# Optimization experiments

Measured on AMD Instinct MI355X. Metric: run time of the kernel, lower is better.

Reference implementation:

```python
import jax, jax.numpy as jnp
import numpy as np

N_NODES = 100000
N_EDGES = 1600000
D_IN = 128
D_HID = 128
D_OUT = 10
N_GRAPHS = 512


def setup_inputs() -> dict:
    key = jax.random.key(0)
    ks = jax.random.split(key, 12)
    x = jax.random.normal(ks[0], (N_NODES, D_IN), dtype=jnp.float32)
    edge_index = jax.random.randint(ks[1], (2, N_EDGES), 0, N_NODES, dtype=jnp.int64)
    batch = jnp.sort(jax.random.randint(ks[2], (N_NODES,), 0, N_GRAPHS, dtype=jnp.int64))
    s = 1.0 / np.sqrt(D_HID)
    W0 = jax.random.normal(ks[3], (D_HID, D_IN), dtype=jnp.float32) * s
    b0 = jax.random.normal(ks[4], (D_HID,), dtype=jnp.float32) * s
    W1 = jax.random.normal(ks[5], (D_HID, D_HID), dtype=jnp.float32) * s
    b1 = jax.random.normal(ks[6], (D_HID,), dtype=jnp.float32) * s
    W2 = jax.random.normal(ks[7], (D_HID, D_HID), dtype=jnp.float32) * s
    b2 = jax.random.normal(ks[8], (D_HID,), dtype=jnp.float32) * s
    Wg = jax.random.normal(ks[9], (D_OUT, D_HID), dtype=jnp.float32) * s
    bg = jax.random.normal(ks[10], (D_OUT,), dtype=jnp.float32) * s
    return {"x": x, "edge_index": edge_index, "batch": batch,
            "W0": W0, "b0": b0, "W1": W1, "b1": b1, "W2": W2, "b2": b2,
            "Wg": Wg, "bg": bg}


def _gin_conv(x, src, dst, W, b):
    # GINConv with eps=0: Linear(x + sum_{j in N(i)} x_j)
    agg = jax.ops.segment_sum(x[src], dst, num_segments=N_NODES)  # [N, d]
    return (x + agg) @ W.T + b


def reference(x, edge_index, batch, W0, b0, W1, b1, W2, b2, Wg, bg):
    src, dst = edge_index[0], edge_index[1]
    h = jax.nn.relu(_gin_conv(x, src, dst, W0, b0))
    h = jax.nn.relu(_gin_conv(h, src, dst, W1, b1))
    h = _gin_conv(h, src, dst, W2, b2)
    # global_mean_pool over graph ids
    sums = jax.ops.segment_sum(h, batch, num_segments=N_GRAPHS)            # [G, d]
    counts = jax.ops.segment_sum(jnp.ones((N_NODES,), h.dtype), batch, num_segments=N_GRAPHS)
    pooled = sums / jnp.maximum(counts, 1.0)[:, None]                       # [G, d]
    return pooled @ Wg.T + bg                                               # [G, out]
```

## Files before the change

kernel.cpp:

```cpp
#include <hip/hip_runtime.h>

#define N_NODES 100000
#define N_EDGES 1600000
#define N_GRAPHS 512
#define NBUCK 391
#define EPB 8192
#define NB_BIN ((N_EDGES + EPB - 1) / EPB)
#define CAP 5120

typedef _Float16 half8 __attribute__((ext_vector_type(8)));
typedef float floatx4 __attribute__((ext_vector_type(4)));

union U16 { uint4 u; half8 h; };


__global__ __launch_bounds__(256) void bucket_hist(const int* __restrict__ dst,
                                                   int* __restrict__ gcnt) {
    __shared__ int c[NBUCK];
    int tid = threadIdx.x;
    for (int i = tid; i < NBUCK; i += 256) c[i] = 0;
    __syncthreads();
    int e0 = blockIdx.x * EPB, e1 = min(e0 + EPB, N_EDGES);
    for (int e = e0 + tid; e < e1; e += 256) atomicAdd(&c[dst[e] >> 8], 1);
    __syncthreads();
    for (int i = tid; i < NBUCK; i += 256) { int v = c[i]; if (v) atomicAdd(&gcnt[i], v); }
}

__global__ __launch_bounds__(512) void bucket_scan(const int* __restrict__ gcnt,
                                                   int* __restrict__ boff,
                                                   int* __restrict__ gcur,
                                                   int* __restrict__ off) {
    __shared__ int ws[8];
    int tid = threadIdx.x;
    int v = (tid < NBUCK) ? gcnt[tid] : 0;
    int lane = tid & 63, w = tid >> 6;
    int incl = v;
    #pragma unroll
    for (int s = 1; s < 64; s <<= 1) { int y = __shfl_up(incl, s, 64); if (lane >= s) incl += y; }
    if (lane == 63) ws[w] = incl;
    __syncthreads();
    if (tid < 8) {
        int t = ws[tid];
        #pragma unroll
        for (int s = 1; s < 8; s <<= 1) { int y = __shfl_up(t, s, 64); if (tid >= s) t += y; }
        ws[tid] = t;
    }
    __syncthreads();
    int excl = (w ? ws[w - 1] : 0) + incl - v;
    if (tid < NBUCK) { boff[tid] = excl; gcur[tid] = excl; }
    if (tid == NBUCK - 1) boff[NBUCK] = excl + v;
    if (tid == 0) off[N_NODES] = N_EDGES;
}

__global__ __launch_bounds__(256) void bucket_scatter(const int* __restrict__ src,
                                                      const int* __restrict__ dst,
                                                      int* __restrict__ gcur,
                                                      int2* __restrict__ pairs) {
    __shared__ int cnt[NBUCK];
    __shared__ int base[NBUCK];
    int tid = threadIdx.x;
    for (int i = tid; i < NBUCK; i += 256) cnt[i] = 0;
    __syncthreads();
    int e0 = blockIdx.x * EPB, e1 = min(e0 + EPB, N_EDGES);
    for (int e = e0 + tid; e < e1; e += 256) atomicAdd(&cnt[dst[e] >> 8], 1);
    __syncthreads();
    for (int i = tid; i < NBUCK; i += 256) {
        int v = cnt[i];
        base[i] = v ? atomicAdd(&gcur[i], v) : 0;
        cnt[i] = 0;
    }
    __syncthreads();
    for (int e = e0 + tid; e < e1; e += 256) {
        int d = dst[e], b = d >> 8;
        int r = atomicAdd(&cnt[b], 1);
        pairs[base[b] + r] = make_int2(src[e], d);
    }
}

__global__ __launch_bounds__(256) void bucket_fine(const int2* __restrict__ pairs,
                                                   const int* __restrict__ boff,
                                                   int* __restrict__ off,
                                                   int* __restrict__ srclist) {
    __shared__ int ncnt[256];
    __shared__ int ws[4];
    __shared__ int stage[CAP];
    int tid = threadIdx.x, b = blockIdx.x;
    int eLo = boff[b], eHi = boff[b + 1], m = eHi - eLo;
    ncnt[tid] = 0;
    __syncthreads();
    for (int t = tid; t < m; t += 256) {
        int2 p = pairs[eLo + t];
        atomicAdd(&ncnt[p.y & 255], 1);
    }
    __syncthreads();
    int v = ncnt[tid];
    int lane = tid & 63, w = tid >> 6;
    int incl = v;
    #pragma unroll
    for (int s = 1; s < 64; s <<= 1) { int y = __shfl_up(incl, s, 64); if (lane >= s) incl += y; }
    if (lane == 63) ws[w] = incl;
    __syncthreads();
    if (tid < 4) {
        int t = ws[tid];
        #pragma unroll
        for (int s = 1; s < 4; s <<= 1) { int y = __shfl_up(t, s, 64); if (tid >= s) t += y; }
        ws[tid] = t;
    }
    __syncthreads();
    int excl = (w ? ws[w - 1] : 0) + incl - v;
    int n = (b << 8) + tid;
    if (n < N_NODES) off[n] = eLo + excl;
    __syncthreads();
    ncnt[tid] = excl;
    __syncthreads();
    for (int t = tid; t < m; t += 256) {
        int2 p = pairs[eLo + t];
        int r = atomicAdd(&ncnt[p.y & 255], 1);
        if (r < CAP) stage[r] = p.x;
        else srclist[eLo + r] = p.x;
    }
    __syncthreads();
    int lim = m < CAP ? m : CAP;
    for (int t = tid; t < lim; t += 256) srclist[eLo + t] = stage[t];
}

__global__ __launch_bounds__(256) void convert_f16(const float4* __restrict__ X4,
                                                   uint4* __restrict__ Xh) {
    int t = blockIdx.x * 256 + threadIdx.x;
    if (t >= N_NODES * 16) return;
    float4 a = X4[t * 2], b = X4[t * 2 + 1];
    U16 o;
    o.h[0] = (_Float16)a.x; o.h[1] = (_Float16)a.y;
    o.h[2] = (_Float16)a.z; o.h[3] = (_Float16)a.w;
    o.h[4] = (_Float16)b.x; o.h[5] = (_Float16)b.y;
    o.h[6] = (_Float16)b.z; o.h[7] = (_Float16)b.w;
    Xh[t] = o.u;
}

__global__ __launch_bounds__(64) void pack_w(const float* __restrict__ W0,
                                             const float* __restrict__ W1,
                                             const float* __restrict__ W2,
                                             uint4* __restrict__ Bp) {
    int b = blockIdx.x;
    int layer = b >> 5;
    int r = b & 31;
    int c = r >> 3, f = r & 7;
    const float* W = (layer == 0) ? W0 : (layer == 1) ? W1 : W2;
    int l = threadIdx.x;
    int col = f * 16 + (l & 15);
    int k0 = c * 32 + (l >> 4) * 8;
    U16 o;
    #pragma unroll
    for (int j = 0; j < 8; ++j) o.h[j] = (_Float16)W[col * 128 + k0 + j];
    Bp[layer * 2048 + (c * 8 + f) * 64 + l] = o.u;
}

__global__ __launch_bounds__(256) void agg_f16(const uint4* __restrict__ Xh,
                                               uint4* __restrict__ Ah,
                                               const int* __restrict__ off,
                                               const int* __restrict__ srclist) {
    int t = blockIdx.x * 256 + threadIdx.x;
    int n = t >> 4, c = t & 15;
    if (n >= N_NODES) return;
    int j0 = off[n], j1 = off[n + 1];
    U16 acc; acc.u = Xh[n * 16 + c];
    half8 a = acc.h;
    int j = j0;
    for (; j + 3 < j1; j += 4) {
        int s0 = srclist[j], s1 = srclist[j + 1], s2 = srclist[j + 2], s3 = srclist[j + 3];
        U16 v0, v1, v2, v3;
        v0.u = Xh[s0 * 16 + c];
        v1.u = Xh[s1 * 16 + c];
        v2.u = Xh[s2 * 16 + c];
        v3.u = Xh[s3 * 16 + c];
        a += v0.h; a += v1.h; a += v2.h; a += v3.h;
    }
    for (; j < j1; ++j) {
        U16 v; v.u = Xh[srclist[j] * 16 + c];
        a += v.h;
    }
    U16 o; o.h = a;
    Ah[n * 16 + c] = o.u;
}

__global__ __launch_bounds__(256) void gemm_mfma(const _Float16* __restrict__ Ah,
                                                 const uint4* __restrict__ Bp,
                                                 const float* __restrict__ bias,
                                                 _Float16* __restrict__ H, int doRelu) {
    int tid = threadIdx.x;
    int wid = tid >> 6, lane = tid & 63;
    int nbase = blockIdx.x * 128 + wid * 32;
    int lrow = lane & 15;
    int lk = (lane >> 4) * 8;
    int row0 = min(nbase + lrow, N_NODES - 1);
    int row1 = min(nbase + 16 + lrow, N_NODES - 1);

    floatx4 acc[2][8];
    #pragma unroll
    for (int r = 0; r < 2; ++r)
        #pragma unroll
        for (int f = 0; f < 8; ++f) acc[r][f] = (floatx4)0.f;

    #pragma unroll
    for (int c = 0; c < 4; ++c) {
        U16 a0, a1;
        a0.u = *(const uint4*)(Ah + row0 * 128 + c * 32 + lk);
        a1.u = *(const uint4*)(Ah + row1 * 128 + c * 32 + lk);
        #pragma unroll
        for (int f = 0; f < 8; ++f) {
            U16 b; b.u = Bp[(c * 8 + f) * 64 + lane];
            acc[0][f] = __builtin_amdgcn_mfma_f32_16x16x32_f16(a0.h, b.h, acc[0][f], 0, 0, 0);
            acc[1][f] = __builtin_amdgcn_mfma_f32_16x16x32_f16(a1.h, b.h, acc[1][f], 0, 0, 0);
        }
    }

    int colb = lane & 15;
    int rq = (lane >> 4) * 4;
    #pragma unroll
    for (int f = 0; f < 8; ++f) {
        float bv = bias[f * 16 + colb];
        #pragma unroll
        for (int r = 0; r < 2; ++r) {
            #pragma unroll
            for (int q = 0; q < 4; ++q) {
                int row = nbase + r * 16 + rq + q;
                if (row < N_NODES) {
                    float v = acc[r][f][q] + bv;
                    if (doRelu) v = fmaxf(v, 0.f);
                    H[row * 128 + f * 16 + colb] = (_Float16)v;
                }
            }
        }
    }
}

__device__ __forceinline__ int lower_bound_i(const int* a, int n, int val) {
    int lo = 0, hi = n;
    while (lo < hi) {
        int mid = (lo + hi) >> 1;
        if (a[mid] < val) lo = mid + 1; else hi = mid;
    }
    return lo;
}

__global__ __launch_bounds__(256) void pool_kernel(const uint4* __restrict__ Hh,
                                                   const int* __restrict__ batch,
                                                   const float* __restrict__ Wg,
                                                   const float* __restrict__ bg,
                                                   float* __restrict__ out) {
    __shared__ float p[16 * 128];
    __shared__ float pooled[128];
    int g = blockIdx.x, tid = threadIdx.x;
    int c = tid & 15, r = tid >> 4;
    int lo = lower_bound_i(batch, N_NODES, g);
    int hi = lower_bound_i(batch, N_NODES, g + 1);
    float acc[8] = {0, 0, 0, 0, 0, 0, 0, 0};
    for (int i = lo + r; i < hi; i += 16) {
        U16 v; v.u = Hh[i * 16 + c];
        #pragma unroll
        for (int k = 0; k < 8; ++k) acc[k] += (float)v.h[k];
    }
    #pragma unroll
    for (int k = 0; k < 8; ++k) p[r * 128 + c * 8 + k] = acc[k];
    __syncthreads();
    if (tid < 128) {
        float s = 0.f;
        #pragma unroll
        for (int q = 0; q < 16; ++q) s += p[q * 128 + tid];
        pooled[tid] = s / fmaxf((float)(hi - lo), 1.0f);
    }
    __syncthreads();
    if (tid < 10) {
        float s = bg[tid];
        #pragma unroll 4
        for (int k = 0; k < 128; ++k) s += pooled[k] * Wg[tid * 128 + k];
        out[g * 10 + tid] = s;
    }
}

extern "C" void kernel_launch(void* const* d_in, const int* in_sizes, int n_in,
                              void* d_out, int out_size, void* d_ws, size_t ws_size,
                              hipStream_t stream) {
    const float* x   = (const float*)d_in[0];
    const int*   ei  = (const int*)d_in[1];
    const int*   bat = (const int*)d_in[2];
    const float* W0  = (const float*)d_in[3];
    const float* b0  = (const float*)d_in[4];
    const float* W1  = (const float*)d_in[5];
    const float* b1  = (const float*)d_in[6];
    const float* W2  = (const float*)d_in[7];
    const float* b2  = (const float*)d_in[8];
    const float* Wg  = (const float*)d_in[9];
    const float* bg  = (const float*)d_in[10];
    float* out = (float*)d_out;

    const int* src = ei;
    const int* dst = ei + N_EDGES;

    char* w = (char*)d_ws;
    _Float16* Ah  = (_Float16*)(w);
    _Float16* Hh  = (_Float16*)(w + 25600000);
    char*   regionR = w + 51200000;
    int2*     pairs = (int2*)regionR;
    _Float16* H2h   = (_Float16*)regionR;
    int*    srclist = (int*)(w + 76800000);
    int*    off     = (int*)(w + 83200000);
    uint4*  Bp      = (uint4*)(w + 83600016);
    int*    gcnt    = (int*)(w + 83698320);
    int*    boff    = gcnt + NBUCK + 1;
    int*    gcur    = boff + NBUCK + 2;

    hipMemsetAsync(gcnt, 0, NBUCK * sizeof(int), stream);

    bucket_hist<<<NB_BIN, 256, 0, stream>>>(dst, gcnt);
    bucket_scan<<<1, 512, 0, stream>>>(gcnt, boff, gcur, off);
    bucket_scatter<<<NB_BIN, 256, 0, stream>>>(src, dst, gcur, pairs);
    bucket_fine<<<NBUCK, 256, 0, stream>>>(pairs, boff, off, srclist);

    convert_f16<<<(N_NODES * 16 + 255) / 256, 256, 0, stream>>>((const float4*)x, (uint4*)Hh);
    pack_w<<<96, 64, 0, stream>>>(W0, W1, W2, Bp);

    int aggGrid  = (N_NODES * 16 + 255) / 256;
    int gemmGrid = (N_NODES + 127) / 128;

    agg_f16<<<aggGrid, 256, 0, stream>>>((const uint4*)Hh, (uint4*)Ah, off, srclist);
    gemm_mfma<<<gemmGrid, 256, 0, stream>>>(Ah, Bp, b0, Hh, 1);
    agg_f16<<<aggGrid, 256, 0, stream>>>((const uint4*)Hh, (uint4*)Ah, off, srclist);
    gemm_mfma<<<gemmGrid, 256, 0, stream>>>(Ah, Bp + 2048, b1, Hh, 1);
    agg_f16<<<aggGrid, 256, 0, stream>>>((const uint4*)Hh, (uint4*)Ah, off, srclist);
    gemm_mfma<<<gemmGrid, 256, 0, stream>>>(Ah, Bp + 4096, b2, H2h, 0);

    pool_kernel<<<N_GRAPHS, 256, 0, stream>>>((const uint4*)H2h, bat, Wg, bg, out);
}
```

Before: 345.6 us.

## Fuse neighbor aggregation with MFMA GEMM and drop bucket histogram pass

Merges the gather-sum aggregation and the MFMA linear layer into one kernel per GIN layer, staging aggregated rows in LDS instead of writing and rereading an intermediate buffer. Replaces the separate bucket histogram pass with fixed-capacity bucket slots whose fill counts feed the scan afterwards. This removes global traffic and several launches, but LDS use may reduce occupancy for the latency-bound gather, and fixed bucket capacity assumes no bucket exceeds CAPB edges.

```diff
diff --git a/kernel.cpp b/kernel.cpp
--- a/kernel.cpp
+++ b/kernel.cpp
@@ -6,6 +6,7 @@
 #define NBUCK 391
 #define EPB 8192
 #define NB_BIN ((N_EDGES + EPB - 1) / EPB)
+#define CAPB 4864
 #define CAP 5120
 
 typedef _Float16 half8 __attribute__((ext_vector_type(8)));
@@ -14,42 +15,9 @@
 union U16 { uint4 u; half8 h; };
 
 
-__global__ __launch_bounds__(256) void bucket_hist(const int* __restrict__ dst,
-                                                   int* __restrict__ gcnt) {
-    __shared__ int c[NBUCK];
-    int tid = threadIdx.x;
-    for (int i = tid; i < NBUCK; i += 256) c[i] = 0;
-    __syncthreads();
-    int e0 = blockIdx.x * EPB, e1 = min(e0 + EPB, N_EDGES);
-    for (int e = e0 + tid; e < e1; e += 256) atomicAdd(&c[dst[e] >> 8], 1);
-    __syncthreads();
-    for (int i = tid; i < NBUCK; i += 256) { int v = c[i]; if (v) atomicAdd(&gcnt[i], v); }
-}
-
-__global__ __launch_bounds__(512) void bucket_scan(const int* __restrict__ gcnt,
-                                                   int* __restrict__ boff,
-                                                   int* __restrict__ gcur,
-                                                   int* __restrict__ off) {
-    __shared__ int ws[8];
-    int tid = threadIdx.x;
-    int v = (tid < NBUCK) ? gcnt[tid] : 0;
-    int lane = tid & 63, w = tid >> 6;
-    int incl = v;
-    #pragma unroll
-    for (int s = 1; s < 64; s <<= 1) { int y = __shfl_up(incl, s, 64); if (lane >= s) incl += y; }
-    if (lane == 63) ws[w] = incl;
-    __syncthreads();
-    if (tid < 8) {
-        int t = ws[tid];
-        #pragma unroll
-        for (int s = 1; s < 8; s <<= 1) { int y = __shfl_up(t, s, 64); if (tid >= s) t += y; }
-        ws[tid] = t;
-    }
-    __syncthreads();
-    int excl = (w ? ws[w - 1] : 0) + incl - v;
-    if (tid < NBUCK) { boff[tid] = excl; gcur[tid] = excl; }
-    if (tid == NBUCK - 1) boff[NBUCK] = excl + v;
-    if (tid == 0) off[N_NODES] = N_EDGES;
+__global__ __launch_bounds__(256) void init_cur(int* __restrict__ gcur) {
+    int t = blockIdx.x * 256 + threadIdx.x;
+    if (t < NBUCK) gcur[t] = t * CAPB;
 }
 
 __global__ __launch_bounds__(256) void bucket_scatter(const int* __restrict__ src,
@@ -77,6 +45,31 @@
     }
 }
 
+__global__ __launch_bounds__(512) void bucket_scan(const int* __restrict__ gcur,
+                                                   int* __restrict__ boff,
+                                                   int* __restrict__ off) {
+    __shared__ int ws[8];
+    int tid = threadIdx.x;
+    int v = (tid < NBUCK) ? (gcur[tid] - tid * CAPB) : 0;
+    int lane = tid & 63, w = tid >> 6;
+    int incl = v;
+    #pragma unroll
+    for (int s = 1; s < 64; s <<= 1) { int y = __shfl_up(incl, s, 64); if (lane >= s) incl += y; }
+    if (lane == 63) ws[w] = incl;
+    __syncthreads();
+    if (tid < 8) {
+        int t = ws[tid];
+        #pragma unroll
+        for (int s = 1; s < 8; s <<= 1) { int y = __shfl_up(t, s, 64); if (tid >= s) t += y; }
+        ws[tid] = t;
+    }
+    __syncthreads();
+    int excl = (w ? ws[w - 1] : 0) + incl - v;
+    if (tid < NBUCK) boff[tid] = excl;
+    if (tid == NBUCK - 1) boff[NBUCK] = excl + v;
+    if (tid == 0) off[N_NODES] = N_EDGES;
+}
+
 __global__ __launch_bounds__(256) void bucket_fine(const int2* __restrict__ pairs,
                                                    const int* __restrict__ boff,
                                                    int* __restrict__ off,
@@ -85,11 +78,12 @@
     __shared__ int ws[4];
     __shared__ int stage[CAP];
     int tid = threadIdx.x, b = blockIdx.x;
-    int eLo = boff[b], eHi = boff[b + 1], m = eHi - eLo;
+    int eLo = boff[b], m = boff[b + 1] - eLo;
+    int sb = b * CAPB;
     ncnt[tid] = 0;
     __syncthreads();
     for (int t = tid; t < m; t += 256) {
-        int2 p = pairs[eLo + t];
+        int2 p = pairs[sb + t];
         atomicAdd(&ncnt[p.y & 255], 1);
     }
     __syncthreads();
@@ -114,7 +108,7 @@
     ncnt[tid] = excl;
     __syncthreads();
     for (int t = tid; t < m; t += 256) {
-        int2 p = pairs[eLo + t];
+        int2 p = pairs[sb + t];
         int r = atomicAdd(&ncnt[p.y & 255], 1);
         if (r < CAP) stage[r] = p.x;
         else srclist[eLo + r] = p.x;
@@ -155,62 +149,74 @@
     Bp[layer * 2048 + (c * 8 + f) * 64 + l] = o.u;
 }
 
-__global__ __launch_bounds__(256) void agg_f16(const uint4* __restrict__ Xh,
-                                               uint4* __restrict__ Ah,
-                                               const int* __restrict__ off,
-                                               const int* __restrict__ srclist) {
-    int t = blockIdx.x * 256 + threadIdx.x;
-    int n = t >> 4, c = t & 15;
-    if (n >= N_NODES) return;
-    int j0 = off[n], j1 = off[n + 1];
-    U16 acc; acc.u = Xh[n * 16 + c];
-    half8 a = acc.h;
-    int j = j0;
-    for (; j + 3 < j1; j += 4) {
-        int s0 = srclist[j], s1 = srclist[j + 1], s2 = srclist[j + 2], s3 = srclist[j + 3];
-        U16 v0, v1, v2, v3;
-        v0.u = Xh[s0 * 16 + c];
-        v1.u = Xh[s1 * 16 + c];
-        v2.u = Xh[s2 * 16 + c];
-        v3.u = Xh[s3 * 16 + c];
-        a += v0.h; a += v1.h; a += v2.h; a += v3.h;
-    }
-    for (; j < j1; ++j) {
-        U16 v; v.u = Xh[srclist[j] * 16 + c];
-        a += v.h;
-    }
-    U16 o; o.h = a;
-    Ah[n * 16 + c] = o.u;
-}
-
-__global__ __launch_bounds__(256) void gemm_mfma(const _Float16* __restrict__ Ah,
+#define LDSW 136
+
+__global__ __launch_bounds__(256) void gin_layer(const uint4* __restrict__ X4,
                                                  const uint4* __restrict__ Bp,
                                                  const float* __restrict__ bias,
-                                                 _Float16* __restrict__ H, int doRelu) {
+                                                 _Float16* __restrict__ H,
+                                                 const int* __restrict__ off,
+                                                 const int* __restrict__ srclist,
+                                                 int doRelu) {
+    __shared__ ushort lds[128 * LDSW];
     int tid = threadIdx.x;
+    int g = tid >> 4;
+    int c = tid & 15;
+    int n0 = blockIdx.x * 128;
+
+    #pragma unroll 1
+    for (int rr = 0; rr < 8; ++rr) {
+        int r = g * 8 + rr;
+        int nc = min(n0 + r, N_NODES - 1);
+        int j0 = off[nc], j1 = off[nc + 1];
+        U16 a; a.u = X4[(size_t)nc * 16 + c];
+        half8 acc = a.h;
+        int j = j0;
+        for (; j + 8 <= j1; j += 8) {
+            int s0 = srclist[j],     s1 = srclist[j + 1], s2 = srclist[j + 2], s3 = srclist[j + 3];
+            int s4 = srclist[j + 4], s5 = srclist[j + 5], s6 = srclist[j + 6], s7 = srclist[j + 7];
+            U16 v0, v1, v2, v3, v4, v5, v6, v7;
+            v0.u = X4[(size_t)s0 * 16 + c];
+            v1.u = X4[(size_t)s1 * 16 + c];
+            v2.u = X4[(size_t)s2 * 16 + c];
+            v3.u = X4[(size_t)s3 * 16 + c];
+            v4.u = X4[(size_t)s4 * 16 + c];
+            v5.u = X4[(size_t)s5 * 16 + c];
+            v6.u = X4[(size_t)s6 * 16 + c];
+            v7.u = X4[(size_t)s7 * 16 + c];
+            acc += v0.h; acc += v1.h; acc += v2.h; acc += v3.h;
+            acc += v4.h; acc += v5.h; acc += v6.h; acc += v7.h;
+        }
+        for (; j < j1; ++j) {
+            U16 v; v.u = X4[(size_t)srclist[j] * 16 + c];
+            acc += v.h;
+        }
+        U16 o; o.h = acc;
+        *(uint4*)&lds[r * LDSW + c * 8] = o.u;
+    }
+    __syncthreads();
+
     int wid = tid >> 6, lane = tid & 63;
-    int nbase = blockIdx.x * 128 + wid * 32;
+    int rbase = wid * 32;
     int lrow = lane & 15;
     int lk = (lane >> 4) * 8;
-    int row0 = min(nbase + lrow, N_NODES - 1);
-    int row1 = min(nbase + 16 + lrow, N_NODES - 1);
-
-    floatx4 acc[2][8];
+
+    floatx4 acc2[2][8];
     #pragma unroll
     for (int r = 0; r < 2; ++r)
         #pragma unroll
-        for (int f = 0; f < 8; ++f) acc[r][f] = (floatx4)0.f;
-
-    #pragma unroll
-    for (int c = 0; c < 4; ++c) {
+        for (int f = 0; f < 8; ++f) acc2[r][f] = (floatx4)0.f;
+
+    #pragma unroll
+    for (int c4 = 0; c4 < 4; ++c4) {
         U16 a0, a1;
-        a0.u = *(const uint4*)(Ah + row0 * 128 + c * 32 + lk);
-        a1.u = *(const uint4*)(Ah + row1 * 128 + c * 32 + lk);
+        a0.u = *(const uint4*)&lds[(rbase + lrow) * LDSW + c4 * 32 + lk];
+        a1.u = *(const uint4*)&lds[(rbase + 16 + lrow) * LDSW + c4 * 32 + lk];
         #pragma unroll
         for (int f = 0; f < 8; ++f) {
-            U16 b; b.u = Bp[(c * 8 + f) * 64 + lane];
-            acc[0][f] = __builtin_amdgcn_mfma_f32_16x16x32_f16(a0.h, b.h, acc[0][f], 0, 0, 0);
-            acc[1][f] = __builtin_amdgcn_mfma_f32_16x16x32_f16(a1.h, b.h, acc[1][f], 0, 0, 0);
+            U16 b; b.u = Bp[(c4 * 8 + f) * 64 + lane];
+            acc2[0][f] = __builtin_amdgcn_mfma_f32_16x16x32_f16(a0.h, b.h, acc2[0][f], 0, 0, 0);
+            acc2[1][f] = __builtin_amdgcn_mfma_f32_16x16x32_f16(a1.h, b.h, acc2[1][f], 0, 0, 0);
         }
     }
 
@@ -223,11 +229,11 @@
         for (int r = 0; r < 2; ++r) {
             #pragma unroll
             for (int q = 0; q < 4; ++q) {
-                int row = nbase + r * 16 + rq + q;
+                int row = n0 + rbase + r * 16 + rq + q;
                 if (row < N_NODES) {
-                    float v = acc[r][f][q] + bv;
+                    float v = acc2[r][f][q] + bv;
                     if (doRelu) v = fmaxf(v, 0.f);
-                    H[row * 128 + f * 16 + colb] = (_Float16)v;
+                    H[(size_t)row * 128 + f * 16 + colb] = (_Float16)v;
                 }
             }
         }
@@ -298,37 +304,28 @@
     const int* dst = ei + N_EDGES;
 
     char* w = (char*)d_ws;
-    _Float16* Ah  = (_Float16*)(w);
-    _Float16* Hh  = (_Float16*)(w + 25600000);
-    char*   regionR = w + 51200000;
-    int2*     pairs = (int2*)regionR;
-    _Float16* H2h   = (_Float16*)regionR;
+    _Float16* P0 = (_Float16*)(w);
+    _Float16* P1 = (_Float16*)(w + 25600000);
+    _Float16* P2 = (_Float16*)(w + 51200000);
+    int2*   pairs   = (int2*)(w + 25600000);
     int*    srclist = (int*)(w + 76800000);
     int*    off     = (int*)(w + 83200000);
-    uint4*  Bp      = (uint4*)(w + 83600016);
-    int*    gcnt    = (int*)(w + 83698320);
-    int*    boff    = gcnt + NBUCK + 1;
-    int*    gcur    = boff + NBUCK + 2;
-
-    hipMemsetAsync(gcnt, 0, NBUCK * sizeof(int), stream);
-
-    bucket_hist<<<NB_BIN, 256, 0, stream>>>(dst, gcnt);
-    bucket_scan<<<1, 512, 0, stream>>>(gcnt, boff, gcur, off);
+    uint4*  Bp      = (uint4*)(w + 83700000);
+    int*    gcur    = (int*)(w + 83900000);
+    int*    boff    = gcur + NBUCK + 1;
+
+    init_cur<<<2, 256, 0, stream>>>(gcur);
     bucket_scatter<<<NB_BIN, 256, 0, stream>>>(src, dst, gcur, pairs);
+    bucket_scan<<<1, 512, 0, stream>>>(gcur, boff, off);
     bucket_fine<<<NBUCK, 256, 0, stream>>>(pairs, boff, off, srclist);
 
-    convert_f16<<<(N_NODES * 16 + 255) / 256, 256, 0, stream>>>((const float4*)x, (uint4*)Hh);
+    convert_f16<<<(N_NODES * 16 + 255) / 256, 256, 0, stream>>>((const float4*)x, (uint4*)P0);
     pack_w<<<96, 64, 0, stream>>>(W0, W1, W2, Bp);
 
-    int aggGrid  = (N_NODES * 16 + 255) / 256;
-    int gemmGrid = (N_NODES + 127) / 128;
-
-    agg_f16<<<aggGrid, 256, 0, stream>>>((const uint4*)Hh, (uint4*)Ah, off, srclist);
-    gemm_mfma<<<gemmGrid, 256, 0, stream>>>(Ah, Bp, b0, Hh, 1);
-    agg_f16<<<aggGrid, 256, 0, stream>>>((const uint4*)Hh, (uint4*)Ah, off, srclist);
-    gemm_mfma<<<gemmGrid, 256, 0, stream>>>(Ah, Bp + 2048, b1, Hh, 1);
-    agg_f16<<<aggGrid, 256, 0, stream>>>((const uint4*)Hh, (uint4*)Ah, off, srclist);
-    gemm_mfma<<<gemmGrid, 256, 0, stream>>>(Ah, Bp + 4096, b2, H2h, 0);
-
-    pool_kernel<<<N_GRAPHS, 256, 0, stream>>>((const uint4*)H2h, bat, Wg, bg, out);
-}
+    int grid = (N_NODES + 127) / 128;
+    gin_layer<<<grid, 256, 0, stream>>>((const uint4*)P0, Bp, b0, P1, off, srclist, 1);
+    gin_layer<<<grid, 256, 0, stream>>>((const uint4*)P1, Bp + 2048, b1, P2, off, srclist, 1);
+    gin_layer<<<grid, 256, 0, stream>>>((const uint4*)P2, Bp + 4096, b2, P0, off, srclist, 0);
+
+    pool_kernel<<<N_GRAPHS, 256, 0, stream>>>((const uint4*)P0, bat, Wg, bg, out);
+}
```

New measurement: 446.5 us. +29.2%, slower.

## Fuse preprocessing into one kernel with fixed-capacity buckets and packed pairs

Applied to the files above, without the earlier changes.

Merges the f16 conversion, edge bucket scatter and weight packing into a single prep kernel. The separate histogram pass is dropped by giving each bucket a fixed-capacity slot region (CAPB). Edge pairs are packed into 32-bit words (17-bit src, 8-bit local dst) to halve pair traffic. The aggregation loop is unrolled to 8 gathers, and ping-pong feature buffers replace the in-place reuse. This saves launches and one pass over dst, but overflows if any bucket exceeds CAPB edges, which holds only for roughly uniform degree distributions.

```diff
diff --git a/kernel.cpp b/kernel.cpp
--- a/kernel.cpp
+++ b/kernel.cpp
@@ -5,34 +5,82 @@
 #define N_GRAPHS 512
 #define NBUCK 391
 #define EPB 8192
-#define NB_BIN ((N_EDGES + EPB - 1) / EPB)
+#define NB_SCAT ((N_EDGES + EPB - 1) / EPB)
+#define CAPB 4864
 #define CAP 5120
+
+#define CONV_BLKS 6250
+#define PACK_BLKS 24
+#define PREP_BLKS (CONV_BLKS + NB_SCAT + PACK_BLKS)
 
 typedef _Float16 half8 __attribute__((ext_vector_type(8)));
 typedef float floatx4 __attribute__((ext_vector_type(4)));
 
 union U16 { uint4 u; half8 h; };
 
-
-__global__ __launch_bounds__(256) void bucket_hist(const int* __restrict__ dst,
-                                                   int* __restrict__ gcnt) {
-    __shared__ int c[NBUCK];
+__global__ __launch_bounds__(256) void prep_kernel(const float4* __restrict__ X4,
+                                                   uint4* __restrict__ Xh,
+                                                   const int* __restrict__ src,
+                                                   const int* __restrict__ dst,
+                                                   int* __restrict__ gcur,
+                                                   unsigned* __restrict__ pairs,
+                                                   const float* __restrict__ W0,
+                                                   const float* __restrict__ W1,
+                                                   const float* __restrict__ W2,
+                                                   uint4* __restrict__ Bp) {
+    int bid = blockIdx.x;
     int tid = threadIdx.x;
-    for (int i = tid; i < NBUCK; i += 256) c[i] = 0;
-    __syncthreads();
-    int e0 = blockIdx.x * EPB, e1 = min(e0 + EPB, N_EDGES);
-    for (int e = e0 + tid; e < e1; e += 256) atomicAdd(&c[dst[e] >> 8], 1);
-    __syncthreads();
-    for (int i = tid; i < NBUCK; i += 256) { int v = c[i]; if (v) atomicAdd(&gcnt[i], v); }
-}
-
-__global__ __launch_bounds__(512) void bucket_scan(const int* __restrict__ gcnt,
+    if (bid < CONV_BLKS) {
+        int t = bid * 256 + tid;
+        float4 a = X4[t * 2], b = X4[t * 2 + 1];
+        U16 o;
+        o.h[0] = (_Float16)a.x; o.h[1] = (_Float16)a.y;
+        o.h[2] = (_Float16)a.z; o.h[3] = (_Float16)a.w;
+        o.h[4] = (_Float16)b.x; o.h[5] = (_Float16)b.y;
+        o.h[6] = (_Float16)b.z; o.h[7] = (_Float16)b.w;
+        Xh[t] = o.u;
+    } else if (bid < CONV_BLKS + NB_SCAT) {
+        __shared__ int cnt[NBUCK];
+        __shared__ int base[NBUCK];
+        int sb = bid - CONV_BLKS;
+        for (int i = tid; i < NBUCK; i += 256) cnt[i] = 0;
+        __syncthreads();
+        int e0 = sb * EPB, e1 = min(e0 + EPB, N_EDGES);
+        for (int e = e0 + tid; e < e1; e += 256) atomicAdd(&cnt[dst[e] >> 8], 1);
+        __syncthreads();
+        for (int i = tid; i < NBUCK; i += 256) {
+            int v = cnt[i];
+            base[i] = i * CAPB + (v ? atomicAdd(&gcur[i], v) : 0);
+            cnt[i] = 0;
+        }
+        __syncthreads();
+        for (int e = e0 + tid; e < e1; e += 256) {
+            int d = dst[e], b = d >> 8;
+            int r = atomicAdd(&cnt[b], 1);
+            pairs[base[b] + r] = (unsigned)src[e] | ((unsigned)(d & 255) << 17);
+        }
+    } else {
+        int slice = (bid - CONV_BLKS - NB_SCAT) * 4 + (tid >> 6);
+        int l = tid & 63;
+        int layer = slice >> 5;
+        int r = slice & 31;
+        int c = r >> 3, f = r & 7;
+        const float* W = (layer == 0) ? W0 : (layer == 1) ? W1 : W2;
+        int col = f * 16 + (l & 15);
+        int k0 = c * 32 + (l >> 4) * 8;
+        U16 o;
+        #pragma unroll
+        for (int j = 0; j < 8; ++j) o.h[j] = (_Float16)W[col * 128 + k0 + j];
+        Bp[layer * 2048 + (c * 8 + f) * 64 + l] = o.u;
+    }
+}
+
+__global__ __launch_bounds__(512) void bucket_scan(const int* __restrict__ gcur,
                                                    int* __restrict__ boff,
-                                                   int* __restrict__ gcur,
                                                    int* __restrict__ off) {
     __shared__ int ws[8];
     int tid = threadIdx.x;
-    int v = (tid < NBUCK) ? gcnt[tid] : 0;
+    int v = (tid < NBUCK) ? gcur[tid] : 0;
     int lane = tid & 63, w = tid >> 6;
     int incl = v;
     #pragma unroll
@@ -47,37 +95,12 @@
     }
     __syncthreads();
     int excl = (w ? ws[w - 1] : 0) + incl - v;
-    if (tid < NBUCK) { boff[tid] = excl; gcur[tid] = excl; }
+    if (tid < NBUCK) boff[tid] = excl;
     if (tid == NBUCK - 1) boff[NBUCK] = excl + v;
     if (tid == 0) off[N_NODES] = N_EDGES;
 }
 
-__global__ __launch_bounds__(256) void bucket_scatter(const int* __restrict__ src,
-                                                      const int* __restrict__ dst,
-                                                      int* __restrict__ gcur,
-                                                      int2* __restrict__ pairs) {
-    __shared__ int cnt[NBUCK];
-    __shared__ int base[NBUCK];
-    int tid = threadIdx.x;
-    for (int i = tid; i < NBUCK; i += 256) cnt[i] = 0;
-    __syncthreads();
-    int e0 = blockIdx.x * EPB, e1 = min(e0 + EPB, N_EDGES);
-    for (int e = e0 + tid; e < e1; e += 256) atomicAdd(&cnt[dst[e] >> 8], 1);
-    __syncthreads();
-    for (int i = tid; i < NBUCK; i += 256) {
-        int v = cnt[i];
-        base[i] = v ? atomicAdd(&gcur[i], v) : 0;
-        cnt[i] = 0;
-    }
-    __syncthreads();
-    for (int e = e0 + tid; e < e1; e += 256) {
-        int d = dst[e], b = d >> 8;
-        int r = atomicAdd(&cnt[b], 1);
-        pairs[base[b] + r] = make_int2(src[e], d);
-    }
-}
-
-__global__ __launch_bounds__(256) void bucket_fine(const int2* __restrict__ pairs,
+__global__ __launch_bounds__(256) void bucket_fine(const unsigned* __restrict__ pairs,
                                                    const int* __restrict__ boff,
                                                    int* __restrict__ off,
                                                    int* __restrict__ srclist) {
@@ -85,12 +108,13 @@
     __shared__ int ws[4];
     __shared__ int stage[CAP];
     int tid = threadIdx.x, b = blockIdx.x;
-    int eLo = boff[b], eHi = boff[b + 1], m = eHi - eLo;
+    int eLo = boff[b], m = boff[b + 1] - eLo;
+    int sb = b * CAPB;
     ncnt[tid] = 0;
     __syncthreads();
     for (int t = tid; t < m; t += 256) {
-        int2 p = pairs[eLo + t];
-        atomicAdd(&ncnt[p.y & 255], 1);
+        unsigned p = pairs[sb + t];
+        atomicAdd(&ncnt[(p >> 17) & 255], 1);
     }
     __syncthreads();
     int v = ncnt[tid];
@@ -114,45 +138,15 @@
     ncnt[tid] = excl;
     __syncthreads();
     for (int t = tid; t < m; t += 256) {
-        int2 p = pairs[eLo + t];
-        int r = atomicAdd(&ncnt[p.y & 255], 1);
-        if (r < CAP) stage[r] = p.x;
-        else srclist[eLo + r] = p.x;
+        unsigned p = pairs[sb + t];
+        int r = atomicAdd(&ncnt[(p >> 17) & 255], 1);
+        int s = (int)(p & 0x1FFFFu);
+        if (r < CAP) stage[r] = s;
+        else srclist[eLo + r] = s;
     }
     __syncthreads();
     int lim = m < CAP ? m : CAP;
     for (int t = tid; t < lim; t += 256) srclist[eLo + t] = stage[t];
-}
-
-__global__ __launch_bounds__(256) void convert_f16(const float4* __restrict__ X4,
-                                                   uint4* __restrict__ Xh) {
-    int t = blockIdx.x * 256 + threadIdx.x;
-    if (t >= N_NODES * 16) return;
-    float4 a = X4[t * 2], b = X4[t * 2 + 1];
-    U16 o;
-    o.h[0] = (_Float16)a.x; o.h[1] = (_Float16)a.y;
-    o.h[2] = (_Float16)a.z; o.h[3] = (_Float16)a.w;
-    o.h[4] = (_Float16)b.x; o.h[5] = (_Float16)b.y;
-    o.h[6] = (_Float16)b.z; o.h[7] = (_Float16)b.w;
-    Xh[t] = o.u;
-}
-
-__global__ __launch_bounds__(64) void pack_w(const float* __restrict__ W0,
-                                             const float* __restrict__ W1,
-                                             const float* __restrict__ W2,
-                                             uint4* __restrict__ Bp) {
-    int b = blockIdx.x;
-    int layer = b >> 5;
-    int r = b & 31;
-    int c = r >> 3, f = r & 7;
-    const float* W = (layer == 0) ? W0 : (layer == 1) ? W1 : W2;
-    int l = threadIdx.x;
-    int col = f * 16 + (l & 15);
-    int k0 = c * 32 + (l >> 4) * 8;
-    U16 o;
-    #pragma unroll
-    for (int j = 0; j < 8; ++j) o.h[j] = (_Float16)W[col * 128 + k0 + j];
-    Bp[layer * 2048 + (c * 8 + f) * 64 + l] = o.u;
 }
 
 __global__ __launch_bounds__(256) void agg_f16(const uint4* __restrict__ Xh,
@@ -163,24 +157,30 @@
     int n = t >> 4, c = t & 15;
     if (n >= N_NODES) return;
     int j0 = off[n], j1 = off[n + 1];
-    U16 acc; acc.u = Xh[n * 16 + c];
+    U16 acc; acc.u = Xh[(size_t)n * 16 + c];
     half8 a = acc.h;
     int j = j0;
-    for (; j + 3 < j1; j += 4) {
-        int s0 = srclist[j], s1 = srclist[j + 1], s2 = srclist[j + 2], s3 = srclist[j + 3];
-        U16 v0, v1, v2, v3;
-        v0.u = Xh[s0 * 16 + c];
-        v1.u = Xh[s1 * 16 + c];
-        v2.u = Xh[s2 * 16 + c];
-        v3.u = Xh[s3 * 16 + c];
+    for (; j + 8 <= j1; j += 8) {
+        int s0 = srclist[j],     s1 = srclist[j + 1], s2 = srclist[j + 2], s3 = srclist[j + 3];
+        int s4 = srclist[j + 4], s5 = srclist[j + 5], s6 = srclist[j + 6], s7 = srclist[j + 7];
+        U16 v0, v1, v2, v3, v4, v5, v6, v7;
+        v0.u = Xh[(size_t)s0 * 16 + c];
+        v1.u = Xh[(size_t)s1 * 16 + c];
+        v2.u = Xh[(size_t)s2 * 16 + c];
+        v3.u = Xh[(size_t)s3 * 16 + c];
+        v4.u = Xh[(size_t)s4 * 16 + c];
+        v5.u = Xh[(size_t)s5 * 16 + c];
+        v6.u = Xh[(size_t)s6 * 16 + c];
+        v7.u = Xh[(size_t)s7 * 16 + c];
         a += v0.h; a += v1.h; a += v2.h; a += v3.h;
+        a += v4.h; a += v5.h; a += v6.h; a += v7.h;
     }
     for (; j < j1; ++j) {
-        U16 v; v.u = Xh[srclist[j] * 16 + c];
+        U16 v; v.u = Xh[(size_t)srclist[j] * 16 + c];
         a += v.h;
     }
     U16 o; o.h = a;
-    Ah[n * 16 + c] = o.u;
+    Ah[(size_t)n * 16 + c] = o.u;
 }
 
 __global__ __launch_bounds__(256) void gemm_mfma(const _Float16* __restrict__ Ah,
@@ -204,8 +204,8 @@
     #pragma unroll
     for (int c = 0; c < 4; ++c) {
         U16 a0, a1;
-        a0.u = *(const uint4*)(Ah + row0 * 128 + c * 32 + lk);
-        a1.u = *(const uint4*)(Ah + row1 * 128 + c * 32 + lk);
+        a0.u = *(const uint4*)(Ah + (size_t)row0 * 128 + c * 32 + lk);
+        a1.u = *(const uint4*)(Ah + (size_t)row1 * 128 + c * 32 + lk);
         #pragma unroll
         for (int f = 0; f < 8; ++f) {
             U16 b; b.u = Bp[(c * 8 + f) * 64 + lane];
@@ -227,7 +227,7 @@
                 if (row < N_NODES) {
                     float v = acc[r][f][q] + bv;
                     if (doRelu) v = fmaxf(v, 0.f);
-                    H[row * 128 + f * 16 + colb] = (_Float16)v;
+                    H[(size_t)row * 128 + f * 16 + colb] = (_Float16)v;
                 }
             }
         }
@@ -256,7 +256,7 @@
     int hi = lower_bound_i(batch, N_NODES, g + 1);
     float acc[8] = {0, 0, 0, 0, 0, 0, 0, 0};
     for (int i = lo + r; i < hi; i += 16) {
-        U16 v; v.u = Hh[i * 16 + c];
+        U16 v; v.u = Hh[(size_t)i * 16 + c];
         #pragma unroll
         for (int k = 0; k < 8; ++k) acc[k] += (float)v.h[k];
     }
@@ -298,37 +298,34 @@
     const int* dst = ei + N_EDGES;
 
     char* w = (char*)d_ws;
-    _Float16* Ah  = (_Float16*)(w);
-    _Float16* Hh  = (_Float16*)(w + 25600000);
-    char*   regionR = w + 51200000;
-    int2*     pairs = (int2*)regionR;
-    _Float16* H2h   = (_Float16*)regionR;
-    int*    srclist = (int*)(w + 76800000);
-    int*    off     = (int*)(w + 83200000);
-    uint4*  Bp      = (uint4*)(w + 83600016);
-    int*    gcnt    = (int*)(w + 83698320);
-    int*    boff    = gcnt + NBUCK + 1;
-    int*    gcur    = boff + NBUCK + 2;
-
-    hipMemsetAsync(gcnt, 0, NBUCK * sizeof(int), stream);
-
-    bucket_hist<<<NB_BIN, 256, 0, stream>>>(dst, gcnt);
-    bucket_scan<<<1, 512, 0, stream>>>(gcnt, boff, gcur, off);
-    bucket_scatter<<<NB_BIN, 256, 0, stream>>>(src, dst, gcur, pairs);
+    _Float16* Ah    = (_Float16*)(w);
+    unsigned* pairs = (unsigned*)(w);
+    _Float16* P0    = (_Float16*)(w + 25600000);
+    _Float16* P1    = (_Float16*)(w + 51200000);
+    _Float16* P2    = (_Float16*)(w + 76800000);
+    int*    srclist = (int*)(w + 102400000);
+    int*    off     = (int*)(w + 108800000);
+    uint4*  Bp      = (uint4*)(w + 109300000);
+    int*    gcur    = (int*)(w + 109450000);
+    int*    boff    = gcur + NBUCK + 1;
+
+    hipMemsetAsync(gcur, 0, NBUCK * sizeof(int), stream);
+
+    prep_kernel<<<PREP_BLKS, 256, 0, stream>>>((const float4*)x, (uint4*)P0,
+                                               src, dst, gcur, pairs,
+                                               W0, W1, W2, Bp);
+    bucket_scan<<<1, 512, 0, stream>>>(gcur, boff, off);
     bucket_fine<<<NBUCK, 256, 0, stream>>>(pairs, boff, off, srclist);
-
-    convert_f16<<<(N_NODES * 16 + 255) / 256, 256, 0, stream>>>((const float4*)x, (uint4*)Hh);
-    pack_w<<<96, 64, 0, stream>>>(W0, W1, W2, Bp);
 
     int aggGrid  = (N_NODES * 16 + 255) / 256;
     int gemmGrid = (N_NODES + 127) / 128;
 
-    agg_f16<<<aggGrid, 256, 0, stream>>>((const uint4*)Hh, (uint4*)Ah, off, srclist);
-    gemm_mfma<<<gemmGrid, 256, 0, stream>>>(Ah, Bp, b0, Hh, 1);
-    agg_f16<<<aggGrid, 256, 0, stream>>>((const uint4*)Hh, (uint4*)Ah, off, srclist);
-    gemm_mfma<<<gemmGrid, 256, 0, stream>>>(Ah, Bp + 2048, b1, Hh, 1);
-    agg_f16<<<aggGrid, 256, 0, stream>>>((const uint4*)Hh, (uint4*)Ah, off, srclist);
-    gemm_mfma<<<gemmGrid, 256, 0, stream>>>(Ah, Bp + 4096, b2, H2h, 0);
-
-    pool_kernel<<<N_GRAPHS, 256, 0, stream>>>((const uint4*)H2h, bat, Wg, bg, out);
-}
+    agg_f16<<<aggGrid, 256, 0, stream>>>((const uint4*)P0, (uint4*)Ah, off, srclist);
+    gemm_mfma<<<gemmGrid, 256, 0, stream>>>(Ah, Bp, b0, P1, 1);
+    agg_f16<<<aggGrid, 256, 0, stream>>>((const uint4*)P1, (uint4*)Ah, off, srclist);
+    gemm_mfma<<<gemmGrid, 256, 0, stream>>>(Ah, Bp + 2048, b1, P2, 1);
+    agg_f16<<<aggGrid, 256, 0, stream>>>((const uint4*)P2, (uint4*)Ah, off, srclist);
+    gemm_mfma<<<gemmGrid, 256, 0, stream>>>(Ah, Bp + 4096, b2, P0, 0);
+
+    pool_kernel<<<N_GRAPHS, 256, 0, stream>>>((const uint4*)P0, bat, Wg, bg, out);
+}
```

After: 340.6 us. No clear change (-1.4%).
